# Performance work log

Measured on AMD Instinct MI355X. Metric: run time of the kernel, lower is better.

Reference implementation:

```python
import jax, jax.numpy as jnp
from jax import lax
import numpy as np

T, B, D = 2048, 16, 1024
INIT_ALPHA_BIAS = 2.0
INIT_D_G = 0.5
INIT_B_G = 0.0


def setup_inputs() -> dict:
    key = jax.random.key(0)
    k_x, k_wa, k_wx = jax.random.split(key, 3)
    scale = 1.0 / np.sqrt(D)  # xavier-ish init for [D,D] weights
    return {
        "x": jax.random.normal(k_x, (T, B, D), dtype=jnp.float32),
        "h0": jnp.zeros((B, D), dtype=jnp.float32),
        "W_alpha": jax.random.normal(k_wa, (D, D), dtype=jnp.float32) * scale,
        "b_alpha": jnp.full((D,), INIT_ALPHA_BIAS, dtype=jnp.float32),
        "W_x": jax.random.normal(k_wx, (D, D), dtype=jnp.float32) * scale,
        "b_v": jnp.zeros((D,), dtype=jnp.float32),
        "d_g": jnp.full((D,), INIT_D_G, dtype=jnp.float32),
        "b_g": jnp.full((D,), INIT_B_G, dtype=jnp.float32),
    }


def reference(x, h0, W_alpha, b_alpha, W_x, b_v, d_g, b_g):
    # Precompute both input projections for all timesteps (one big GEMM each).
    # x @ W.T + b, matching torch Linear-style layout W[dim_out, dim_in].
    alpha_all = jax.nn.sigmoid(jnp.einsum("tbd,ed->tbe", x, W_alpha) + b_alpha)  # [T,B,D]
    v_raw_all = jnp.tanh(jnp.einsum("tbd,ed->tbe", x, W_x) + b_v)                # [T,B,D]

    def step(h_prev, inp):
        alpha, v_raw = inp
        g = jax.nn.sigmoid(d_g * h_prev + b_g)        # self-gating on previous state
        v = v_raw * g
        h_new = alpha * h_prev + (1.0 - alpha) * v
        out = h_new * h_new * jax.nn.sigmoid(h_new)   # h * silu(h)
        return h_new, (out, h_new)

    _, (output, h_seq) = lax.scan(step, h0, (alpha_all, v_raw_all))
    h = jnp.concatenate([h0[None], h_seq], axis=0)    # [T+1,B,D]
    return output, h
```

## Files before the change

kernel.cpp:

```cpp
#include <hip/hip_runtime.h>

typedef unsigned short u16;
typedef unsigned int u32;

#define T_ 2048
#define B_ 16
#define D_ 1024
constexpr int MM = T_ * B_;
constexpr int KK = D_;
constexpr int NN = 2 * D_;
constexpr int BD = B_ * D_;
constexpr int BM = 128, BN = 128, BK = 32;

typedef __bf16 bf16x8 __attribute__((ext_vector_type(8)));
typedef float f32x4 __attribute__((ext_vector_type(4)));

typedef __attribute__((address_space(3))) u32 lds_u32_t;
typedef __attribute__((address_space(1))) u32 gbl_u32_t;

__device__ __forceinline__ void gld16(void* lds, const void* g) {
    __builtin_amdgcn_global_load_lds((const gbl_u32_t*)g, (lds_u32_t*)lds, 16, 0, 0);
}

__device__ __forceinline__ float fast_sig(float x) {
    return __builtin_amdgcn_rcpf(1.0f + __expf(-x));
}

__device__ __forceinline__ float fast_exp2(float x) {
#if __has_builtin(__builtin_amdgcn_exp2f)
    return __builtin_amdgcn_exp2f(x);
#else
    return exp2f(x);
#endif
}

__device__ inline void split1(float f, u16& h, u16& l) {
    u32 u = __float_as_uint(f);
    h = (u16)(u >> 16);
    float fh = __uint_as_float(u & 0xffff0000u);
    float r = f - fh;
    l = (u16)(__float_as_uint(r) >> 16);
}

__global__ __launch_bounds__(256) void split_kernel(
    const float* __restrict__ src, u16* __restrict__ hi, u16* __restrict__ lo, int n4)
{
    int i = blockIdx.x * 256 + threadIdx.x;
    if (i >= n4) return;
    float4 v = ((const float4*)src)[i];
    u16 h0, h1, h2, h3, l0, l1, l2, l3;
    split1(v.x, h0, l0); split1(v.y, h1, l1);
    split1(v.z, h2, l2); split1(v.w, h3, l3);
    ushort4 hv; hv.x = h0; hv.y = h1; hv.z = h2; hv.w = h3;
    ushort4 lv; lv.x = l0; lv.y = l1; lv.z = l2; lv.w = l3;
    ((ushort4*)hi)[i] = hv;
    ((ushort4*)lo)[i] = lv;
}

__global__ __launch_bounds__(256) void gemm_dual(
    const u16* __restrict__ xhi, const u16* __restrict__ xlo,
    const u16* __restrict__ whi, const u16* __restrict__ wlo,
    const float* __restrict__ ba, const float* __restrict__ bv,
    float* __restrict__ out_ptr, float* __restrict__ h_ptr)
{
    __shared__ u16 Ah[BM][BK];
    __shared__ u16 Al[BM][BK];
    __shared__ u16 Bh[BN][BK];
    __shared__ u16 Bl[BN][BK];

    const int tid  = threadIdx.x;
    const int m0   = blockIdx.y * BM;
    const int n0   = blockIdx.x * BN;
    const int wave = tid >> 6, lane = tid & 63;
    const int wm = (wave & 1) << 6;
    const int wn = (wave >> 1) << 6;
    const int fm = lane & 15, quad = lane >> 4;
    const int wb = wave << 5;
    const int rl = lane >> 2;
    const int cl = (lane & 3) << 3;

    f32x4 acc[4][4] = {};

    for (int k0 = 0; k0 < KK; k0 += BK) {
        size_t ga = (size_t)(m0 + wb + rl) * KK + k0 + cl;
        size_t gb = (size_t)(n0 + wb + rl) * KK + k0 + cl;
        gld16(&Ah[wb][0],      xhi + ga);
        gld16(&Ah[wb + 16][0], xhi + ga + (size_t)16 * KK);
        gld16(&Al[wb][0],      xlo + ga);
        gld16(&Al[wb + 16][0], xlo + ga + (size_t)16 * KK);
        gld16(&Bh[wb][0],      whi + gb);
        gld16(&Bh[wb + 16][0], whi + gb + (size_t)16 * KK);
        gld16(&Bl[wb][0],      wlo + gb);
        gld16(&Bl[wb + 16][0], wlo + gb + (size_t)16 * KK);
        __syncthreads();

        bf16x8 ah[4], al[4], bh[4], bl[4];
        #pragma unroll
        for (int i = 0; i < 4; ++i) {
            ah[i] = *(const bf16x8*)&Ah[wm + i * 16 + fm][quad * 8];
            al[i] = *(const bf16x8*)&Al[wm + i * 16 + fm][quad * 8];
            bh[i] = *(const bf16x8*)&Bh[wn + i * 16 + fm][quad * 8];
            bl[i] = *(const bf16x8*)&Bl[wn + i * 16 + fm][quad * 8];
        }
        #pragma unroll
        for (int mi = 0; mi < 4; ++mi) {
            #pragma unroll
            for (int ni = 0; ni < 4; ++ni) {
                acc[mi][ni] = __builtin_amdgcn_mfma_f32_16x16x32_bf16(ah[mi], bh[ni], acc[mi][ni], 0, 0, 0);
                acc[mi][ni] = __builtin_amdgcn_mfma_f32_16x16x32_bf16(ah[mi], bl[ni], acc[mi][ni], 0, 0, 0);
                acc[mi][ni] = __builtin_amdgcn_mfma_f32_16x16x32_bf16(al[mi], bh[ni], acc[mi][ni], 0, 0, 0);
            }
        }
        __syncthreads();
    }

    const bool is_alpha = (n0 < D_);
    #pragma unroll
    for (int mi = 0; mi < 4; ++mi) {
        #pragma unroll
        for (int ni = 0; ni < 4; ++ni) {
            const int nglob = n0 + wn + ni * 16 + fm;
            #pragma unroll
            for (int r = 0; r < 4; ++r) {
                const int mglob = m0 + wm + mi * 16 + quad * 4 + r;
                float z = acc[mi][ni][r];
                if (is_alpha) {
                    z += ba[nglob];
                    float s = 1.0f / (1.0f + __expf(-z));
                    h_ptr[(size_t)BD + (size_t)mglob * D_ + nglob] = s;
                } else {
                    int nn = nglob - D_;
                    z += bv[nn];
                    out_ptr[(size_t)mglob * D_ + nn] = tanhf(z);
                }
            }
        }
    }
}

#define SCAN_BODY(A_, V_) do {                                        \
    float a_  = (A_);                                                 \
    float vr_ = (V_);                                                 \
    float e_  = fast_exp2(__builtin_fmaf(ndg, h, nbg));               \
    float g_  = __builtin_amdgcn_rcpf(1.0f + e_);                     \
    float v_  = vr_ * g_;                                             \
    h = __builtin_fmaf(a_, h - v_, v_);                               \
    float e2_ = fast_exp2(h * -1.44269504088896f);                    \
    float sg_ = __builtin_amdgcn_rcpf(1.0f + e2_);                    \
    __builtin_nontemporal_store(h * h * sg_, po + (size_t)t * BD);    \
    __builtin_nontemporal_store(h, ph + (size_t)t * BD);              \
    ++t;                                                              \
} while (0)

__global__ __launch_bounds__(64) void scan_kernel(
    const float* __restrict__ alpha_p,
    const float* __restrict__ vraw_p,
    float* __restrict__ out_p,
    float* __restrict__ hout_p,
    float* __restrict__ h0_dst,
    const float* __restrict__ h0,
    const float* __restrict__ d_g, const float* __restrict__ b_g)
{
    const int i = blockIdx.x * 64 + threadIdx.x;
    const int d = i & (D_ - 1);
    constexpr float L2E = 1.44269504088896f;
    const float ndg = -d_g[d] * L2E;
    const float nbg = -b_g[d] * L2E;
    float h = h0[i];
    h0_dst[i] = h;

    const float* pa = alpha_p + i;
    const float* pv = vraw_p + i;
    float* po = out_p + i;
    float* ph = hout_p + i;

    constexpr int PF = 16;
    constexpr int NC = T_ / PF;
    float a0[PF], v0[PF], a1[PF], v1[PF];

    #pragma unroll
    for (int p = 0; p < PF; ++p) {
        a0[p] = pa[(size_t)p * BD];
        v0[p] = pv[(size_t)p * BD];
    }

    int t = 0;
    for (int c = 0; c < NC / 2 - 1; ++c) {
        #pragma unroll
        for (int p = 0; p < PF; ++p) {
            a1[p] = pa[(size_t)(t + PF + p) * BD];
            v1[p] = pv[(size_t)(t + PF + p) * BD];
        }
        #pragma unroll
        for (int p = 0; p < PF; ++p) SCAN_BODY(a0[p], v0[p]);
        #pragma unroll
        for (int p = 0; p < PF; ++p) {
            a0[p] = pa[(size_t)(t + PF + p) * BD];
            v0[p] = pv[(size_t)(t + PF + p) * BD];
        }
        #pragma unroll
        for (int p = 0; p < PF; ++p) SCAN_BODY(a1[p], v1[p]);
    }
    #pragma unroll
    for (int p = 0; p < PF; ++p) {
        a1[p] = pa[(size_t)(t + PF + p) * BD];
        v1[p] = pv[(size_t)(t + PF + p) * BD];
    }
    #pragma unroll
    for (int p = 0; p < PF; ++p) SCAN_BODY(a0[p], v0[p]);
    #pragma unroll
    for (int p = 0; p < PF; ++p) SCAN_BODY(a1[p], v1[p]);
}

extern "C" void kernel_launch(void* const* d_in, const int* in_sizes, int n_in,
                              void* d_out, int out_size, void* d_ws, size_t ws_size,
                              hipStream_t stream) {
    const float* x  = (const float*)d_in[0];
    const float* h0 = (const float*)d_in[1];
    const float* Wa = (const float*)d_in[2];
    const float* ba = (const float*)d_in[3];
    const float* Wx = (const float*)d_in[4];
    const float* bv = (const float*)d_in[5];
    const float* dg = (const float*)d_in[6];
    const float* bg = (const float*)d_in[7];

    float* out_ptr = (float*)d_out;
    float* h_ptr   = out_ptr + (size_t)T_ * BD;

    u16* xhi = (u16*)d_ws;
    u16* xlo = xhi + (size_t)MM * KK;
    u16* whi = xlo + (size_t)MM * KK;
    u16* wlo = whi + (size_t)NN * KK;

    int n4x = MM * KK / 4;
    split_kernel<<<n4x / 256, 256, 0, stream>>>(x, xhi, xlo, n4x);
    int n4w = D_ * D_ / 4;
    split_kernel<<<n4w / 256, 256, 0, stream>>>(Wa, whi, wlo, n4w);
    split_kernel<<<n4w / 256, 256, 0, stream>>>(Wx, whi + (size_t)D_ * KK, wlo + (size_t)D_ * KK, n4w);

    dim3 grid(NN / BN, MM / BM);
    gemm_dual<<<grid, 256, 0, stream>>>(xhi, xlo, whi, wlo, ba, bv, out_ptr, h_ptr);

    scan_kernel<<<BD / 64, 64, 0, stream>>>(
        h_ptr + BD, out_ptr,
        out_ptr, h_ptr + BD, h_ptr,
        h0, dg, bg);
}
```

Measured before the change: 1.024 ms.

## Stream scan inputs through a 4-deep LDS ring with async global-to-LDS loads

The scan kernel no longer prefetches alpha and v_raw into two register arrays of 16. It now issues `global_load_lds` copies into a 4-stage LDS ring buffer (8 timesteps per stage). Explicit `s_waitcnt vmcnt` values track how many loads and nontemporal stores may still be in flight. The goal is to keep more memory requests outstanding per wave and to cut register pressure in this latency-bound, low-occupancy recurrence. The risk is that the hand-counted vmcnt thresholds must exactly match the compiler's instruction emission; if the stores or loads are reordered or counted differently, a stage could be read before its data arrives.

Measured after the change: 997.6 us. -2.6%, faster.

```diff
diff --git a/kernel.cpp b/kernel.cpp
--- a/kernel.cpp
+++ b/kernel.cpp
@@ -20,10 +20,6 @@
 
 __device__ __forceinline__ void gld16(void* lds, const void* g) {
     __builtin_amdgcn_global_load_lds((const gbl_u32_t*)g, (lds_u32_t*)lds, 16, 0, 0);
-}
-
-__device__ __forceinline__ float fast_sig(float x) {
-    return __builtin_amdgcn_rcpf(1.0f + __expf(-x));
 }
 
 __device__ __forceinline__ float fast_exp2(float x) {
@@ -138,19 +134,7 @@
     }
 }
 
-#define SCAN_BODY(A_, V_) do {                                        \
-    float a_  = (A_);                                                 \
-    float vr_ = (V_);                                                 \
-    float e_  = fast_exp2(__builtin_fmaf(ndg, h, nbg));               \
-    float g_  = __builtin_amdgcn_rcpf(1.0f + e_);                     \
-    float v_  = vr_ * g_;                                             \
-    h = __builtin_fmaf(a_, h - v_, v_);                               \
-    float e2_ = fast_exp2(h * -1.44269504088896f);                    \
-    float sg_ = __builtin_amdgcn_rcpf(1.0f + e2_);                    \
-    __builtin_nontemporal_store(h * h * sg_, po + (size_t)t * BD);    \
-    __builtin_nontemporal_store(h, ph + (size_t)t * BD);              \
-    ++t;                                                              \
-} while (0)
+#define WAITV(N) asm volatile("s_waitcnt vmcnt(" #N ")" ::: "memory")
 
 __global__ __launch_bounds__(64) void scan_kernel(
     const float* __restrict__ alpha_p,
@@ -161,55 +145,72 @@
     const float* __restrict__ h0,
     const float* __restrict__ d_g, const float* __restrict__ b_g)
 {
-    const int i = blockIdx.x * 64 + threadIdx.x;
-    const int d = i & (D_ - 1);
+    constexpr int PF = 8;
+    constexpr int NC = T_ / PF;
+    __shared__ float ring[4][2][PF][64];
+
+    const int lane = threadIdx.x;
+    const int c0   = blockIdx.x * 64;
+    const int i    = c0 + lane;
+    const int d    = i & (D_ - 1);
     constexpr float L2E = 1.44269504088896f;
     const float ndg = -d_g[d] * L2E;
     const float nbg = -b_g[d] * L2E;
     float h = h0[i];
     h0_dst[i] = h;
 
-    const float* pa = alpha_p + i;
-    const float* pv = vraw_p + i;
-    float* po = out_p + i;
-    float* ph = hout_p + i;
-
-    constexpr int PF = 16;
-    constexpr int NC = T_ / PF;
-    float a0[PF], v0[PF], a1[PF], v1[PF];
-
-    #pragma unroll
-    for (int p = 0; p < PF; ++p) {
-        a0[p] = pa[(size_t)p * BD];
-        v0[p] = pv[(size_t)p * BD];
+    const float* po = out_p + i;
+    const float* dummy = po; (void)dummy;
+    float* pov = out_p + i;
+    float* phv = hout_p + i;
+
+    const size_t gcol = (size_t)c0 + (size_t)((lane & 15) << 2);
+    const int trow = lane >> 4;
+
+#define ISSUE(c_) do {                                                        \
+    const int b_ = (c_) & 3;                                                  \
+    const size_t t0_ = (size_t)((c_) * PF + trow) * BD + gcol;                \
+    gld16(&ring[b_][0][0][0], alpha_p + t0_);                                 \
+    gld16(&ring[b_][0][4][0], alpha_p + t0_ + (size_t)4 * BD);                \
+    gld16(&ring[b_][1][0][0], vraw_p  + t0_);                                 \
+    gld16(&ring[b_][1][4][0], vraw_p  + t0_ + (size_t)4 * BD);                \
+} while (0)
+
+#define COMPUTE(c_) do {                                                      \
+    const int b_ = (c_) & 3;                                                  \
+    _Pragma("unroll")                                                         \
+    for (int p = 0; p < PF; ++p) {                                            \
+        float a_  = ring[b_][0][p][lane];                                     \
+        float vr_ = ring[b_][1][p][lane];                                     \
+        float e_  = fast_exp2(__builtin_fmaf(ndg, h, nbg));                   \
+        float g_  = __builtin_amdgcn_rcpf(1.0f + e_);                         \
+        float v_  = vr_ * g_;                                                 \
+        h = __builtin_fmaf(a_, h - v_, v_);                                   \
+        float sg_ = __builtin_amdgcn_rcpf(1.0f + fast_exp2(h * -L2E));        \
+        const size_t off_ = (size_t)((c_) * PF + p) * BD;                     \
+        __builtin_nontemporal_store(h * h * sg_, pov + off_);                 \
+        __builtin_nontemporal_store(h, phv + off_);                           \
+    }                                                                         \
+} while (0)
+
+    ISSUE(0); ISSUE(1); ISSUE(2);
+
+    ISSUE(3); WAITV(8);  COMPUTE(0);
+    ISSUE(4); WAITV(24); COMPUTE(1);
+    ISSUE(5); WAITV(40); COMPUTE(2);
+
+    for (int c = 3; c < NC - 3; ++c) {
+        ISSUE(c + 3);
+        WAITV(56);
+        COMPUTE(c);
     }
 
-    int t = 0;
-    for (int c = 0; c < NC / 2 - 1; ++c) {
-        #pragma unroll
-        for (int p = 0; p < PF; ++p) {
-            a1[p] = pa[(size_t)(t + PF + p) * BD];
-            v1[p] = pv[(size_t)(t + PF + p) * BD];
-        }
-        #pragma unroll
-        for (int p = 0; p < PF; ++p) SCAN_BODY(a0[p], v0[p]);
-        #pragma unroll
-        for (int p = 0; p < PF; ++p) {
-            a0[p] = pa[(size_t)(t + PF + p) * BD];
-            v0[p] = pv[(size_t)(t + PF + p) * BD];
-        }
-        #pragma unroll
-        for (int p = 0; p < PF; ++p) SCAN_BODY(a1[p], v1[p]);
-    }
-    #pragma unroll
-    for (int p = 0; p < PF; ++p) {
-        a1[p] = pa[(size_t)(t + PF + p) * BD];
-        v1[p] = pv[(size_t)(t + PF + p) * BD];
-    }
-    #pragma unroll
-    for (int p = 0; p < PF; ++p) SCAN_BODY(a0[p], v0[p]);
-    #pragma unroll
-    for (int p = 0; p < PF; ++p) SCAN_BODY(a1[p], v1[p]);
+    WAITV(52); COMPUTE(NC - 3);
+    WAITV(48); COMPUTE(NC - 2);
+    WAITV(44); COMPUTE(NC - 1);
+
+#undef ISSUE
+#undef COMPUTE
 }
 
 extern "C" void kernel_launch(void* const* d_in, const int* in_sizes, int n_in,
```
